# Kernel tuning notes

Measured on AMD Instinct MI355X. Metric: run time of the kernel, lower is better.

## Reference

```python
import jax, jax.numpy as jnp
import numpy as np

B, S, D, H = 4, 2048, 1024, 16
DK = D // H

def setup_inputs() -> dict:
    key = jax.random.key(0)
    ks = jax.random.split(key, 13)
    std = 1.0 / np.sqrt(D)
    inp = {
        'query': jax.random.normal(ks[0], (B, S, D), jnp.float32),
        'key':   jax.random.normal(ks[1], (B, S, D), jnp.float32),
        'value': jax.random.normal(ks[2], (B, S, D), jnp.float32),
        'mask':  jax.random.randint(ks[3], (B, 1, S), 0, 2, jnp.int32),
        'Wq': jax.random.normal(ks[4], (D, D), jnp.float32) * std,
        'bq': jnp.zeros((D,), jnp.float32),
        'Wk': jax.random.normal(ks[5], (D, D), jnp.float32) * std,
        'bk': jnp.zeros((D,), jnp.float32),
        'Wv': jax.random.normal(ks[6], (D, D), jnp.float32) * std,
        'bv': jnp.zeros((D,), jnp.float32),
        'Wo': jax.random.normal(ks[7], (D, D), jnp.float32) * std,
        'bo': jnp.zeros((D,), jnp.float32),
    }
    return inp

def reference(query, key, value, mask, Wq, bq, Wk, bk, Wv, bv, Wo, bo):
    # QKV projections (torch Linear: x @ W.T + b), reshape to [B,H,S,DK]
    def proj(x, W, b):
        y = x @ W.T + b
        return y.reshape(B, S, H, DK).transpose(0, 2, 1, 3)
    q = proj(query, Wq, bq)
    k = proj(key, Wk, bk)
    v = proj(value, Wv, bv)
    scores = jnp.einsum('bhqd,bhkd->bhqk', q, k) / jnp.sqrt(jnp.float32(DK))
    # mask [B,1,S] -> unsqueeze head dim -> [B,1,1,S], broadcast over h,q
    m = mask[:, None, :, :]  # [B,1,1,S]
    scores = jnp.where(m == 0, jnp.float32(-1e9), scores)
    p = jax.nn.softmax(scores, axis=-1)  # dropout omitted (eval mode)
    x = jnp.einsum('bhqk,bhkd->bhqd', p, v)
    x = x.transpose(0, 2, 1, 3).reshape(B, S, D)
    return x @ Wo.T + bo
```

## Files before the change

### kernel.cpp

```cpp
#include <hip/hip_runtime.h>

typedef unsigned short u16;
typedef unsigned int u32;
typedef __bf16 bf16x8 __attribute__((ext_vector_type(8)));
typedef float f32x4 __attribute__((ext_vector_type(4)));
typedef u16 u16x8 __attribute__((ext_vector_type(8)));
typedef u16 u16x4 __attribute__((ext_vector_type(4)));

typedef __attribute__((address_space(1))) const unsigned char gc_u8;
typedef __attribute__((address_space(3))) unsigned char lds_u8;

__device__ inline void gload16(const void* g, void* l) {
    __builtin_amdgcn_global_load_lds((gc_u8*)g, (lds_u8*)l, 16, 0, 0);
}
__device__ inline u16 f2bf(float f) {
    union { __bf16 h; u16 u; } c; c.h = (__bf16)f; return c.u;
}
__device__ inline float bf2f(u16 u) {
    union { u16 u[2]; float f; } c; c.u[0] = 0; c.u[1] = u; return c.f;
}
__device__ inline void hard_barrier() {
    __builtin_amdgcn_sched_barrier(0);
    __builtin_amdgcn_s_barrier();
    __builtin_amdgcn_sched_barrier(0);
}
#define WAIT_LGKM0() asm volatile("s_waitcnt lgkmcnt(0)" ::: "memory")
#define WAIT_VMCNT(n) asm volatile("s_waitcnt vmcnt(" #n ")" ::: "memory")

__global__ __launch_bounds__(256) void cvt4(const float* __restrict__ s0,
                                            const float* __restrict__ s1,
                                            const float* __restrict__ s2,
                                            const float* __restrict__ s3,
                                            u16* __restrict__ d0, u16* __restrict__ d1,
                                            u16* __restrict__ d2, u16* __restrict__ d3,
                                            int n) {
    const int y = blockIdx.y;
    const float* src = (y == 0) ? s0 : (y == 1) ? s1 : (y == 2) ? s2 : s3;
    u16* dst = (y == 0) ? d0 : (y == 1) ? d1 : (y == 2) ? d2 : d3;
    int i = (blockIdx.x * 256 + threadIdx.x) * 4;
    if (i < n) {
        float4 f = *reinterpret_cast<const float4*>(src + i);
        u16x4 u = { f2bf(f.x), f2bf(f.y), f2bf(f.z), f2bf(f.w) };
        *reinterpret_cast<u16x4*>(dst + i) = u;
    }
}

__global__ __launch_bounds__(256) void build_dtok(const int* __restrict__ mask,
                                                  int* __restrict__ dtok,
                                                  int* __restrict__ NbA) {
    __shared__ u32 W[64];
    __shared__ u32 Wpre[65];
    const int b = blockIdx.x, t = threadIdx.x;
    const int* mrow = mask + b * 2048;
    if (t < 64) {
        u32 wv = 0;
#pragma unroll 8
        for (int j = 0; j < 32; j++) wv |= (mrow[t * 32 + j] ? 1u : 0u) << j;
        W[t] = wv;
    }
    __syncthreads();
    if (t == 0) {
        u32 s = 0;
        for (int i = 0; i < 64; i++) { Wpre[i] = s; s += __popc(W[i]); }
        Wpre[64] = s;
        NbA[b] = (int)s;
    }
    __syncthreads();
    const int Nb = (int)Wpre[64];
    const int pad = (Nb + 127) & ~127;
#pragma unroll
    for (int i = 0; i < 8; i++) {
        const int s = t * 8 + i;
        const u32 word = W[s >> 5];
        const int pre = (int)Wpre[s >> 5] + __popc(word & ((1u << (s & 31)) - 1u));
        int v;
        if ((word >> (s & 31)) & 1u) {
            v = pre;
        } else {
            const int slot = Nb + (s - pre);
            v = (slot < pad) ? -(slot + 2) : -1;
        }
        dtok[b * 2048 + s] = v;
    }
}

__global__ __launch_bounds__(256) void gemm_qkv(const float* __restrict__ Aq,
                                                const float* __restrict__ Ak,
                                                const float* __restrict__ Av,
                                                const u16* __restrict__ Bq,
                                                const u16* __restrict__ Bk,
                                                const u16* __restrict__ Bv,
                                                const float* __restrict__ bq,
                                                const float* __restrict__ bk,
                                                const float* __restrict__ bv,
                                                const int* __restrict__ dtok,
                                                u16* __restrict__ Cq,
                                                u16* __restrict__ Ck,
                                                u16* __restrict__ Cvp,
                                                int M, int N, int K) {
    __shared__ __align__(16) float Asf[2][128][32];
    __shared__ __align__(16) u16 Bs[2][128][32];
    const int z = blockIdx.z;
    const float* A = (z == 0) ? Aq : (z == 1) ? Ak : Av;
    const u16* B = (z == 0) ? Bq : (z == 1) ? Bk : Bv;
    const float* bias = (z == 0) ? bq : (z == 1) ? bk : bv;

    const int t = threadIdx.x, lane = t & 63, w = t >> 6;
    const int wr = w >> 1, wc = w & 1;
    const int l15 = lane & 15, l16 = lane >> 4;
    const int nwg = gridDim.x, ntiles = N >> 7;
    const int wg = blockIdx.x, chunk = nwg >> 3;
    const int swz = (wg & 7) * chunk + (wg >> 3);
    const int bm = (swz / ntiles) * 128, bn = (swz % ntiles) * 128;
    const int srow = w * 16 + (lane >> 2);
    const int sgrB = ((lane & 3) ^ ((lane >> 3) & 3)) * 8;
    const int gswB = (l16 ^ ((l15 >> 1) & 3)) * 8;
    const int arsub = lane >> 3;
    const int agr = ((lane & 7) ^ (lane >> 3)) * 4;
    const u16* Bb = B + (size_t)bn * K;

    f32x4 acc[4][4];
#pragma unroll
    for (int i = 0; i < 4; i++)
#pragma unroll
        for (int j = 0; j < 4; j++) acc[i][j] = (f32x4){0.f, 0.f, 0.f, 0.f};

    auto stage = [&](int c, int k0) {
#pragma unroll
        for (int ch = 0; ch < 4; ch++)
            gload16(A + (size_t)(bm + ch * 32 + w * 8 + arsub) * K + k0 + agr,
                    &Asf[c][ch * 32 + w * 8][0]);
        gload16(Bb + (size_t)srow * K + k0 + sgrB,        &Bs[c][w * 16][0]);
        gload16(Bb + (size_t)(64 + srow) * K + k0 + sgrB, &Bs[c][64 + w * 16][0]);
    };

    stage(0, 0);
    __syncthreads();

    const int NS = K >> 5;
    for (int i = 0; i < NS; ++i) {
        const int c = i & 1;
        WAIT_LGKM0();
        hard_barrier();
        if (i + 1 < NS) {
            stage(c ^ 1, (i + 1) * 32);
            WAIT_VMCNT(6);
        } else {
            WAIT_VMCNT(0);
        }
        hard_barrier();

        const int key = l15 & 7;
        bf16x8 afr[4], bfr[4];
#pragma unroll
        for (int mi = 0; mi < 4; mi++) {
            const int rr = wr * 64 + mi * 16 + l15;
            f32x4 lo = *(const f32x4*)&Asf[c][rr][((2 * l16) ^ key) * 4];
            f32x4 hi = *(const f32x4*)&Asf[c][rr][((2 * l16 + 1) ^ key) * 4];
            bf16x8 v;
            v[0] = (__bf16)lo[0]; v[1] = (__bf16)lo[1];
            v[2] = (__bf16)lo[2]; v[3] = (__bf16)lo[3];
            v[4] = (__bf16)hi[0]; v[5] = (__bf16)hi[1];
            v[6] = (__bf16)hi[2]; v[7] = (__bf16)hi[3];
            afr[mi] = v;
        }
#pragma unroll
        for (int ni = 0; ni < 4; ni++)
            bfr[ni] = *(const bf16x8*)&Bs[c][wc * 64 + ni * 16 + l15][gswB];
#pragma unroll
        for (int mi = 0; mi < 4; mi++)
#pragma unroll
            for (int ni = 0; ni < 4; ni++)
                acc[mi][ni] = __builtin_amdgcn_mfma_f32_16x16x32_bf16(
                    afr[mi], bfr[ni], acc[mi][ni], 0, 0, 0);
    }

    int dts[4][4];
    if (z != 0) {
#pragma unroll
        for (int mi = 0; mi < 4; mi++) {
            const int r0 = bm + wr * 64 + mi * 16 + l16 * 4;
#pragma unroll
            for (int r = 0; r < 4; r++) dts[mi][r] = dtok[r0 + r];
        }
    }

#pragma unroll
    for (int ni = 0; ni < 4; ni++) {
        const int col = bn + wc * 64 + ni * 16 + l15;
        const float bv2 = bias[col];
#pragma unroll
        for (int mi = 0; mi < 4; mi++) {
            const int r0 = bm + wr * 64 + mi * 16 + l16 * 4;
            const int bb = r0 >> 11;
            if (z == 0) {
#pragma unroll
                for (int r = 0; r < 4; r++)
                    Cq[(size_t)(r0 + r) * N + col] = f2bf(acc[mi][ni][r] + bv2);
            } else if (z == 1) {
#pragma unroll
                for (int r = 0; r < 4; r++) {
                    const int d = dts[mi][r];
                    if (d >= 0)
                        Ck[((size_t)(bb * 2048 + d)) * 1024 + col] =
                            f2bf(acc[mi][ni][r] + bv2);
                    else if (d != -1)
                        Ck[((size_t)(bb * 2048 + (-d - 2))) * 1024 + col] = 0;
                }
            } else {
                const int hh = col >> 6, dk = col & 63;
                u16* dst = Cvp + (((size_t)(bb * 16 + hh) * 64 + dk) << 11);
#pragma unroll
                for (int r = 0; r < 4; r++) {
                    const int d = dts[mi][r];
                    if (d >= 0) dst[d] = f2bf(acc[mi][ni][r] + bv2);
                    else if (d != -1) dst[-d - 2] = 0;
                }
            }
        }
    }
}

__global__ __launch_bounds__(256) void gemm_out(const u16* __restrict__ A,
                                                const u16* __restrict__ B,
                                                const float* __restrict__ bias,
                                                float* __restrict__ Cv,
                                                int M, int N, int K) {
    __shared__ __align__(16) u16 As[2][128][32];
    __shared__ __align__(16) u16 Bs[2][128][32];
    const int t = threadIdx.x, lane = t & 63, w = t >> 6;
    const int wr = w >> 1, wc = w & 1;
    const int l15 = lane & 15, l16 = lane >> 4;
    const int nwg = gridDim.x, ntiles = N >> 7;
    const int wg = blockIdx.x, chunk = nwg >> 3;
    const int swz = (wg & 7) * chunk + (wg >> 3);
    const int bm = (swz / ntiles) * 128, bn = (swz % ntiles) * 128;
    const int srow = w * 16 + (lane >> 2);
    const int sgrB = ((lane & 3) ^ ((lane >> 3) & 3)) * 8;
    const int gswB = (l16 ^ ((l15 >> 1) & 3)) * 8;
    const u16* Ab = A + (size_t)bm * K;
    const u16* Bb = B + (size_t)bn * K;

    f32x4 acc[4][4];
#pragma unroll
    for (int i = 0; i < 4; i++)
#pragma unroll
        for (int j = 0; j < 4; j++) acc[i][j] = (f32x4){0.f, 0.f, 0.f, 0.f};

    auto stage = [&](int c, int k0) {
        gload16(Ab + (size_t)srow * K + k0 + sgrB,        &As[c][w * 16][0]);
        gload16(Ab + (size_t)(64 + srow) * K + k0 + sgrB, &As[c][64 + w * 16][0]);
        gload16(Bb + (size_t)srow * K + k0 + sgrB,        &Bs[c][w * 16][0]);
        gload16(Bb + (size_t)(64 + srow) * K + k0 + sgrB, &Bs[c][64 + w * 16][0]);
    };

    stage(0, 0);
    __syncthreads();

    const int NS = K >> 5;
    for (int i = 0; i < NS; ++i) {
        const int c = i & 1;
        WAIT_LGKM0();
        hard_barrier();
        if (i + 1 < NS) {
            stage(c ^ 1, (i + 1) * 32);
            WAIT_VMCNT(4);
        } else {
            WAIT_VMCNT(0);
        }
        hard_barrier();

        bf16x8 afr[4], bfr[4];
#pragma unroll
        for (int mi = 0; mi < 4; mi++)
            afr[mi] = *(const bf16x8*)&As[c][wr * 64 + mi * 16 + l15][gswB];
#pragma unroll
        for (int ni = 0; ni < 4; ni++)
            bfr[ni] = *(const bf16x8*)&Bs[c][wc * 64 + ni * 16 + l15][gswB];
#pragma unroll
        for (int mi = 0; mi < 4; mi++)
#pragma unroll
            for (int ni = 0; ni < 4; ni++)
                acc[mi][ni] = __builtin_amdgcn_mfma_f32_16x16x32_bf16(
                    afr[mi], bfr[ni], acc[mi][ni], 0, 0, 0);
    }

#pragma unroll
    for (int ni = 0; ni < 4; ni++) {
        const int col = bn + wc * 64 + ni * 16 + l15;
        const float bv = bias[col];
#pragma unroll
        for (int mi = 0; mi < 4; mi++) {
            const int r0 = bm + wr * 64 + mi * 16 + l16 * 4;
#pragma unroll
            for (int r = 0; r < 4; r++)
                Cv[(size_t)(r0 + r) * N + col] = acc[mi][ni][r] + bv;
        }
    }
}

__global__ __launch_bounds__(256, 2) void attn_fwd(const u16* __restrict__ Q,
                                                   const u16* __restrict__ Kg,
                                                   const u16* __restrict__ Vt,
                                                   const int* __restrict__ NbA,
                                                   u16* __restrict__ O) {
    constexpr int S = 2048, D = 1024;
    __shared__ __align__(16) u16 Kl[2][2][2][64][32];
    __shared__ __align__(16) u16 Vl[2][2][2][64][32];
    __shared__ __align__(16) u16 Pl[4][16][68];
    __shared__ __align__(16) u16 Ml[2048];
    const int t = threadIdx.x, lane = t & 63, w = t >> 6;
    const int l15 = lane & 15, l16 = lane >> 4;
    const int wg = blockIdx.x;
    const int swz = (wg & 7) * 64 + (wg >> 3);
    const int q0 = (swz & 7) * 256, hd = (swz >> 3) & 15, b = swz >> 7;
    const int qb = q0 + w * 64;
    const int srow = w * 16 + (lane >> 2);
    const int sgr = ((lane & 3) ^ ((lane >> 3) & 3)) * 8;
    const int gsw8 = (l16 ^ ((l15 >> 1) & 3)) * 8;

    const int Nb = NbA[b];
    const int nt = (Nb + 127) >> 7;

    const u16* Khead = Kg + (size_t)b * S * D;
    const u16* Vthead = Vt + (size_t)(b * 16 + hd) * 64 * 2048;

    auto stage = [&](int c, int kt) {
#pragma unroll
        for (int kg = 0; kg < 2; kg++) {
            const int k0 = kt + kg * 64;
            gload16(Khead + (size_t)(k0 + srow) * D + hd * 64 + sgr,      &Kl[c][kg][0][w * 16][0]);
            gload16(Khead + (size_t)(k0 + srow) * D + hd * 64 + 32 + sgr, &Kl[c][kg][1][w * 16][0]);
            gload16(Vthead + (size_t)srow * 2048 + k0 + sgr,              &Vl[c][kg][0][w * 16][0]);
            gload16(Vthead + (size_t)srow * 2048 + k0 + 32 + sgr,         &Vl[c][kg][1][w * 16][0]);
        }
    };

    stage(0, 0);
    {
        u16x8 mv;
#pragma unroll
        for (int j = 0; j < 8; j++) mv[j] = (t * 8 + j < Nb) ? (u16)0x3F80 : (u16)0;
        *(u16x8*)&Ml[t * 8] = mv;
    }

    constexpr float QSCALE = 0.125f * 1.44269504f;
    bf16x8 aq[4][2];
#pragma unroll
    for (int qt = 0; qt < 4; qt++)
#pragma unroll
        for (int ks = 0; ks < 2; ks++) {
            const size_t qi = ((size_t)b * S + qb + qt * 16 + l15) * D +
                              hd * 64 + ks * 32 + l16 * 8;
            u16x8 raw = *(const u16x8*)&Q[qi];
            bf16x8 qv;
#pragma unroll
            for (int i = 0; i < 8; i++) qv[i] = (__bf16)(bf2f(raw[i]) * QSCALE);
            aq[qt][ks] = qv;
        }

    f32x4 acc[4][4];
    f32x4 accl[4];
#pragma unroll
    for (int qt = 0; qt < 4; qt++) {
        accl[qt] = (f32x4){0.f, 0.f, 0.f, 0.f};
#pragma unroll
        for (int dt = 0; dt < 4; dt++) acc[qt][dt] = (f32x4){0.f, 0.f, 0.f, 0.f};
    }

    __syncthreads();

    for (int tile = 0; tile < nt; ++tile) {
        const int c = tile & 1;
        const int cur = tile * 128;
        WAIT_LGKM0();
        hard_barrier();
        if (tile + 1 < nt) {
            stage(c ^ 1, cur + 128);
            WAIT_VMCNT(8);
        } else {
            WAIT_VMCNT(0);
        }
        hard_barrier();

#pragma unroll
        for (int kg = 0; kg < 2; kg++) {
            bf16x8 kf0[4], kf1[4], vf0[4], vf1[4];
#pragma unroll
            for (int k4 = 0; k4 < 4; k4++) {
                kf0[k4] = *(const bf16x8*)&Kl[c][kg][0][k4 * 16 + l15][gsw8];
                kf1[k4] = *(const bf16x8*)&Kl[c][kg][1][k4 * 16 + l15][gsw8];
            }
#pragma unroll
            for (int dt = 0; dt < 4; dt++) {
                vf0[dt] = *(const bf16x8*)&Vl[c][kg][0][dt * 16 + l15][gsw8];
                vf1[dt] = *(const bf16x8*)&Vl[c][kg][1][dt * 16 + l15][gsw8];
            }
            const int kbase = cur + kg * 64;
            bf16x8 mv0 = *(const bf16x8*)&Ml[kbase + l16 * 8];
            bf16x8 mv1 = *(const bf16x8*)&Ml[kbase + 32 + l16 * 8];

#pragma unroll
            for (int qt = 0; qt < 4; qt++) {
#pragma unroll
                for (int k4 = 0; k4 < 4; k4++) {
                    f32x4 z = (f32x4){0.f, 0.f, 0.f, 0.f};
                    z = __builtin_amdgcn_mfma_f32_16x16x32_bf16(kf0[k4], aq[qt][0], z, 0, 0, 0);
                    z = __builtin_amdgcn_mfma_f32_16x16x32_bf16(kf1[k4], aq[qt][1], z, 0, 0, 0);
                    u16x4 pk;
#pragma unroll
                    for (int r = 0; r < 4; r++)
                        pk[r] = f2bf(__builtin_amdgcn_exp2f(z[r]));
                    *(u16x4*)&Pl[w][l15][k4 * 16 + l16 * 4] = pk;
                }
                bf16x8 pa0 = *(const bf16x8*)&Pl[w][l15][l16 * 8];
                bf16x8 pa1 = *(const bf16x8*)&Pl[w][l15][32 + l16 * 8];
                accl[qt] = __builtin_amdgcn_mfma_f32_16x16x32_bf16(pa0, mv0, accl[qt], 0, 0, 0);
                accl[qt] = __builtin_amdgcn_mfma_f32_16x16x32_bf16(pa1, mv1, accl[qt], 0, 0, 0);
#pragma unroll
                for (int dt = 0; dt < 4; dt++) {
                    acc[qt][dt] = __builtin_amdgcn_mfma_f32_16x16x32_bf16(
                        pa0, vf0[dt], acc[qt][dt], 0, 0, 0);
                    acc[qt][dt] = __builtin_amdgcn_mfma_f32_16x16x32_bf16(
                        pa1, vf1[dt], acc[qt][dt], 0, 0, 0);
                }
            }
        }
    }

#pragma unroll
    for (int qt = 0; qt < 4; qt++) {
        f32x4 inv;
#pragma unroll
        for (int r = 0; r < 4; r++) inv[r] = 1.f / accl[qt][r];
#pragma unroll
        for (int dt = 0; dt < 4; dt++)
#pragma unroll
            for (int r = 0; r < 4; r++) {
                const int tok = qb + qt * 16 + l16 * 4 + r;
                O[((size_t)b * S + tok) * D + hd * 64 + dt * 16 + l15] =
                    f2bf(acc[qt][dt][r] * inv[r]);
            }
    }
}

extern "C" void kernel_launch(void* const* d_in, const int* in_sizes, int n_in,
                              void* d_out, int out_size, void* d_ws, size_t ws_size,
                              hipStream_t stream) {
    const float* query = (const float*)d_in[0];
    const float* key   = (const float*)d_in[1];
    const float* value = (const float*)d_in[2];
    const int*   mask  = (const int*)d_in[3];
    const float* Wq = (const float*)d_in[4];
    const float* bq = (const float*)d_in[5];
    const float* Wk = (const float*)d_in[6];
    const float* bk = (const float*)d_in[7];
    const float* Wv = (const float*)d_in[8];
    const float* bv = (const float*)d_in[9];
    const float* Wo = (const float*)d_in[10];
    const float* bo = (const float*)d_in[11];
    float* out = (float*)d_out;

    constexpr int S = 2048, D = 1024;
    constexpr size_t MSZ = (size_t)4 * S * D;
    constexpr size_t WSZ = (size_t)D * D;
    const size_t need = 4 * WSZ * 2 + 2 * MSZ * 2 + 8192 * 4 + 64;
    if (ws_size < need) return;

    char* p = (char*)d_ws;
    u16* Wqb = (u16*)p; p += WSZ * 2;
    u16* Wkb = (u16*)p; p += WSZ * 2;
    u16* Wvb = (u16*)p; p += WSZ * 2;
    u16* Wob = (u16*)p; p += WSZ * 2;
    u16* Xb  = (u16*)p; p += MSZ * 2;
    u16* Qb  = (u16*)p; p += MSZ * 2;
    int* dtok = (int*)p; p += 8192 * 4;
    int* NbA = (int*)p; p += 64;
    u16* Kc  = (u16*)d_out;
    u16* Vtc = (u16*)d_out + MSZ;

    cvt4<<<dim3(WSZ / 1024, 4), 256, 0, stream>>>(Wq, Wk, Wv, Wo,
                                                  Wqb, Wkb, Wvb, Wob, (int)WSZ);
    build_dtok<<<4, 256, 0, stream>>>(mask, dtok, NbA);
    gemm_qkv<<<dim3(512, 1, 3), 256, 0, stream>>>(query, key, value,
                                                  Wqb, Wkb, Wvb, bq, bk, bv, dtok,
                                                  Qb, Kc, Vtc, 8192, 1024, 1024);
    attn_fwd<<<512, 256, 0, stream>>>(Qb, Kc, Vtc, NbA, Xb);
    gemm_out<<<512, 256, 0, stream>>>(Xb, Wob, bo, out, 8192, 1024, 1024);
}
```

Baseline: 179.0 us.

## Convert QKV GEMM A tile to bf16 in registers before writing LDS

The QKV projection GEMM no longer copies the fp32 A tile straight into LDS and converts it to bf16 on every fragment read. Instead it loads A into registers, converts it to bf16 once, and writes it to a swizzled bf16 LDS buffer that uses the same layout as B. This removes the redundant per-wave conversions, halves A's LDS footprint and read traffic, and lets A fragments be read with single 16-byte loads. The cost is giving up the asynchronous direct-to-LDS copy for A. The wait on the next tile's A loads now sits before the current tile's MFMAs, so global-load latency may be exposed.

```diff
diff --git a/kernel.cpp b/kernel.cpp
--- a/kernel.cpp
+++ b/kernel.cpp
@@ -98,7 +98,7 @@
                                                 u16* __restrict__ Ck,
                                                 u16* __restrict__ Cvp,
                                                 int M, int N, int K) {
-    __shared__ __align__(16) float Asf[2][128][32];
+    __shared__ __align__(16) u16 As[2][128][32];
     __shared__ __align__(16) u16 Bs[2][128][32];
     const int z = blockIdx.z;
     const float* A = (z == 0) ? Aq : (z == 1) ? Ak : Av;
@@ -112,11 +112,11 @@
     const int wg = blockIdx.x, chunk = nwg >> 3;
     const int swz = (wg & 7) * chunk + (wg >> 3);
     const int bm = (swz / ntiles) * 128, bn = (swz % ntiles) * 128;
+    const int row = t >> 1, cc = (t & 1) * 16;
+    const int akey = (t >> 2) & 3, agb = (t & 1) * 2;
     const int srow = w * 16 + (lane >> 2);
     const int sgrB = ((lane & 3) ^ ((lane >> 3) & 3)) * 8;
     const int gswB = (l16 ^ ((l15 >> 1) & 3)) * 8;
-    const int arsub = lane >> 3;
-    const int agr = ((lane & 7) ^ (lane >> 3)) * 4;
     const u16* Bb = B + (size_t)bn * K;
 
     f32x4 acc[4][4];
@@ -125,45 +125,52 @@
 #pragma unroll
         for (int j = 0; j < 4; j++) acc[i][j] = (f32x4){0.f, 0.f, 0.f, 0.f};
 
-    auto stage = [&](int c, int k0) {
-#pragma unroll
-        for (int ch = 0; ch < 4; ch++)
-            gload16(A + (size_t)(bm + ch * 32 + w * 8 + arsub) * K + k0 + agr,
-                    &Asf[c][ch * 32 + w * 8][0]);
+    float4 f0, f1, f2, f3;
+    auto loadA = [&](int k0) {
+        const float* Ap = A + (size_t)(bm + row) * K + k0 + cc;
+        f0 = *(const float4*)(Ap);
+        f1 = *(const float4*)(Ap + 4);
+        f2 = *(const float4*)(Ap + 8);
+        f3 = *(const float4*)(Ap + 12);
+    };
+    auto cvtwrite = [&](int c) {
+        u16x8 a0 = (u16x8){f2bf(f0.x), f2bf(f0.y), f2bf(f0.z), f2bf(f0.w),
+                           f2bf(f1.x), f2bf(f1.y), f2bf(f1.z), f2bf(f1.w)};
+        u16x8 a1 = (u16x8){f2bf(f2.x), f2bf(f2.y), f2bf(f2.z), f2bf(f2.w),
+                           f2bf(f3.x), f2bf(f3.y), f2bf(f3.z), f2bf(f3.w)};
+        *(u16x8*)&As[c][row][((agb + 0) ^ akey) * 8] = a0;
+        *(u16x8*)&As[c][row][((agb + 1) ^ akey) * 8] = a1;
+    };
+    auto stageB = [&](int c, int k0) {
         gload16(Bb + (size_t)srow * K + k0 + sgrB,        &Bs[c][w * 16][0]);
         gload16(Bb + (size_t)(64 + srow) * K + k0 + sgrB, &Bs[c][64 + w * 16][0]);
     };
 
-    stage(0, 0);
+    loadA(0);
+    stageB(0, 0);
+    WAIT_VMCNT(2);
+    cvtwrite(0);
     __syncthreads();
 
     const int NS = K >> 5;
     for (int i = 0; i < NS; ++i) {
         const int c = i & 1;
+        if (i + 1 < NS) loadA((i + 1) * 32);
         WAIT_LGKM0();
         hard_barrier();
         if (i + 1 < NS) {
-            stage(c ^ 1, (i + 1) * 32);
-            WAIT_VMCNT(6);
+            stageB(c ^ 1, (i + 1) * 32);
+            WAIT_VMCNT(2);
+            cvtwrite(c ^ 1);
         } else {
             WAIT_VMCNT(0);
         }
         hard_barrier();
 
-        const int key = l15 & 7;
         bf16x8 afr[4], bfr[4];
 #pragma unroll
-        for (int mi = 0; mi < 4; mi++) {
-            const int rr = wr * 64 + mi * 16 + l15;
-            f32x4 lo = *(const f32x4*)&Asf[c][rr][((2 * l16) ^ key) * 4];
-            f32x4 hi = *(const f32x4*)&Asf[c][rr][((2 * l16 + 1) ^ key) * 4];
-            bf16x8 v;
-            v[0] = (__bf16)lo[0]; v[1] = (__bf16)lo[1];
-            v[2] = (__bf16)lo[2]; v[3] = (__bf16)lo[3];
-            v[4] = (__bf16)hi[0]; v[5] = (__bf16)hi[1];
-            v[6] = (__bf16)hi[2]; v[7] = (__bf16)hi[3];
-            afr[mi] = v;
-        }
+        for (int mi = 0; mi < 4; mi++)
+            afr[mi] = *(const bf16x8*)&As[c][wr * 64 + mi * 16 + l15][gswB];
 #pragma unroll
         for (int ni = 0; ni < 4; ni++)
             bfr[ni] = *(const bf16x8*)&Bs[c][wc * 64 + ni * 16 + l15][gswB];
```

After: 183.9 us. 2.8% more time.
